# Optimization experiments

Measured on AMD Instinct MI355X. Metric: run time of the kernel, lower is better.

Reference implementation:

```python
import jax, jax.numpy as jnp
import numpy as np

B, C, D = 512, 50000, 256
N_LOADED = 40000


def setup_inputs() -> dict:
    key = jax.random.key(0)
    k1, k2, k3, k4 = jax.random.split(key, 4)
    visual_feats = jax.random.normal(k1, (B, D), dtype=jnp.float32)
    text_feats = jax.random.normal(k2, (C, D), dtype=jnp.float32)
    # sparse multi-hot labels; force class 0 positive for every row so the
    # positive set (intersected with loaded ids) is never empty
    batch_label = (jax.random.uniform(k3, (B, C)) < 0.02).astype(jnp.int32)
    batch_label = batch_label.at[:, 0].set(1)
    # distinct loaded class ids; force id 0 to be loaded
    ids = jax.random.permutation(k4, C)[:N_LOADED].astype(jnp.int32)
    ids = jnp.sort(ids).at[0].set(0)
    return {
        "visual_feats": visual_feats,
        "text_feats": text_feats,
        "batch_label": batch_label,
        "class_ids_loaded": ids,
        "d_space": D,
    }


def reference(visual_feats, text_feats, batch_label, class_ids_loaded, d_space):
    num_classes = text_feats.shape[0]
    # membership mask for loaded class ids (the set() intersection in torch)
    loaded = jnp.zeros((num_classes,), dtype=bool).at[class_ids_loaded].set(True)

    # cosine similarity; note: torch adds 1e-6 eps only to text-feature norms
    v = visual_feats / jnp.linalg.norm(visual_feats, axis=1, keepdims=True)
    t = text_feats / (1e-6 + jnp.linalg.norm(text_feats, axis=1, keepdims=True))
    S = v @ t.T  # [B, C]

    pos = (batch_label != 0) & loaded[None, :]  # ragged positive sets, as mask
    neg = (batch_label == 0) & loaded[None, :]  # ragged negative sets, as mask

    # denominator: sum of exp(sim) over negatives, per row
    denom = jnp.sum(jnp.where(neg, jnp.exp(S), 0.0), axis=1)  # [B]
    n_pos = jnp.sum(pos, axis=1).astype(S.dtype)  # [B]

    # per-row loss: mean over positives of -log(exp(s_p)/denom) = log(denom)-s_p
    per_row = jnp.sum(jnp.where(pos, jnp.log(denom)[:, None] - S, 0.0), axis=1) / n_pos
    return jnp.mean(per_row).reshape(1)
```

## Files before the change

kernel.cpp:

```cpp
#include <hip/hip_runtime.h>
#include <math.h>

#define D_DIM 256
#define TM 128
#define TN 128
#define BK 32
#define NBP 392
#define CBPR 7
#define CBLKS (CBPR * 512)

typedef __attribute__((ext_vector_type(8))) short short8;
typedef __attribute__((ext_vector_type(4))) float floatx4;
typedef unsigned long long u64;

__device__ __forceinline__ unsigned short f2bf(float f) {
    unsigned int u = __float_as_uint(f);
    u += 0x7FFFu + ((u >> 16) & 1u);
    return (unsigned short)(u >> 16);
}

__device__ __forceinline__ void gload16(const void* g, void* lds) {
    __builtin_amdgcn_global_load_lds(
        (const __attribute__((address_space(1))) unsigned int*)g,
        (__attribute__((address_space(3))) unsigned int*)lds, 16, 0, 0);
}

__global__ __launch_bounds__(256) void prep_compress(
    const float* __restrict__ V, const float* __restrict__ T,
    const int* __restrict__ label, const int* __restrict__ ids,
    u64* __restrict__ loadedmask, u64* __restrict__ posmask,
    unsigned short* __restrict__ Vb, unsigned short* __restrict__ Tb,
    float* __restrict__ gaccum, unsigned int* __restrict__ gcount,
    int B, int C, int n_loaded, int WPR) {
    const int bid = blockIdx.x;
    const int tid = threadIdx.x;
    const int lane = tid & 63;

    if (bid < CBLKS) {
        int row = bid / CBPR;
        int sub = bid - row * CBPR;
        int wl  = tid >> 6;
        int w0col = (sub * 4 + wl) * 2048;
        if (w0col >= C) return;
        const int* lp = label + (size_t)row * C;
        int4 v[8];
        #pragma unroll
        for (int r = 0; r < 8; ++r) {
            int c0 = w0col + r * 256 + lane * 4;
            if (c0 < C) {
                v[r] = *(const int4*)(lp + c0);
            } else {
                v[r] = make_int4(0, 0, 0, 0);
            }
        }
        #pragma unroll
        for (int r = 0; r < 8; ++r) {
            unsigned int nib =
                (v[r].x ? 1u : 0u) | (v[r].y ? 2u : 0u) |
                (v[r].z ? 4u : 0u) | (v[r].w ? 8u : 0u);
            u64 wv = (u64)nib << (4 * (lane & 15));
            wv |= __shfl_xor(wv, 1);
            wv |= __shfl_xor(wv, 2);
            wv |= __shfl_xor(wv, 4);
            wv |= __shfl_xor(wv, 8);
            if ((lane & 15) == 0) {
                int wc = ((w0col + r * 256) >> 6) + (lane >> 4);
                if (wc < WPR) posmask[(size_t)row * WPR + wc] = wv;
            }
        }
        return;
    }

    int ptid = (bid - CBLKS) * 256 + tid;
    if (ptid == 0) { *gcount = 0u; *gaccum = 0.f; }
    if (ptid < WPR) {
        int base = ptid << 6;
        int lo = 0, hi = n_loaded;
        while (lo < hi) { int mid = (lo + hi) >> 1; if (ids[mid] < base) lo = mid + 1; else hi = mid; }
        u64 m = 0;
        for (int i = lo; i < n_loaded; ++i) {
            int v = ids[i]; if (v >= base + 64) break;
            m |= 1ull << (v - base);
        }
        loadedmask[ptid] = m;
    }
    int wave = ptid >> 6;
    if (wave >= B + C) return;
    bool isV = wave < B;
    const float* src = isV ? (V + (size_t)wave * D_DIM)
                           : (T + (size_t)(wave - B) * D_DIM);
    float4 x = ((const float4*)src)[lane];
    float ss = x.x * x.x + x.y * x.y + x.z * x.z + x.w * x.w;
    #pragma unroll
    for (int off = 32; off > 0; off >>= 1) ss += __shfl_xor(ss, off);
    float nrm = sqrtf(ss);
    float s = isV ? (1.0f / nrm) : (1.0f / (1e-6f + nrm));
    ushort4 o;
    o.x = f2bf(x.x * s); o.y = f2bf(x.y * s);
    o.z = f2bf(x.z * s); o.w = f2bf(x.w * s);
    unsigned short* dst = isV ? (Vb + (size_t)wave * D_DIM)
                              : (Tb + (size_t)(wave - B) * D_DIM);
    ((ushort4*)dst)[lane] = o;
}

__global__ __launch_bounds__(256) void gemm_fused(
    const unsigned short* __restrict__ Vb, const unsigned short* __restrict__ Tb,
    const u64* __restrict__ posmask, const u64* __restrict__ loadedmask,
    float* __restrict__ denomP, float* __restrict__ posP, int C, int WPR) {
    __shared__ unsigned short As[2][TM * BK];
    __shared__ unsigned short Bs[2][TN * BK];
    __shared__ float sDen[TM], sPos[TM];

    const int tid  = threadIdx.x;
    const int lane = tid & 63;
    const int w    = tid >> 6;
    const int m0 = blockIdx.x * TM;
    const int n0 = blockIdx.y * TN;

    if (tid < TM) { sDen[tid] = 0.f; sPos[tid] = 0.f; }

    const int sra = lane >> 2;
    const int kc  = (lane & 3) * 8;
    int ga  = m0 + w * 32 + sra;
    int gb0 = n0 + w * 32 + sra;
    int gb1 = gb0 + 16;
    if (gb0 >= C) gb0 = C - 1;
    if (gb1 >= C) gb1 = C - 1;
    const unsigned short* gA0 = Vb + (size_t)ga * D_DIM + kc;
    const unsigned short* gA1 = gA0 + (size_t)16 * D_DIM;
    const unsigned short* gB0 = Tb + (size_t)gb0 * D_DIM + kc;
    const unsigned short* gB1 = Tb + (size_t)gb1 * D_DIM + kc;
    const int lofsA = w * 32 * BK;
    const int lofsB = w * 32 * BK;

    const int wm = (w >> 1) * 64;
    const int wn = (w & 1) * 64;
    const int fr = lane & 15;
    const int quad = lane >> 4;

    floatx4 acc[4][4];
    #pragma unroll
    for (int mi = 0; mi < 4; mi++)
        #pragma unroll
        for (int ni = 0; ni < 4; ni++) acc[mi][ni] = (floatx4)0.f;

    gload16(gA0, &As[0][lofsA]);
    gload16(gA1, &As[0][lofsA + 16 * BK]);
    gload16(gB0, &Bs[0][lofsB]);
    gload16(gB1, &Bs[0][lofsB + 16 * BK]);
    __syncthreads();

    #pragma unroll
    for (int kt = 0; kt < D_DIM / BK; ++kt) {
        const int cur = kt & 1;
        if (kt < D_DIM / BK - 1) {
            const int kb = (kt + 1) * BK;
            gload16(gA0 + kb, &As[cur ^ 1][lofsA]);
            gload16(gA1 + kb, &As[cur ^ 1][lofsA + 16 * BK]);
            gload16(gB0 + kb, &Bs[cur ^ 1][lofsB]);
            gload16(gB1 + kb, &Bs[cur ^ 1][lofsB + 16 * BK]);
        }
        short8 af[4], bf[4];
        #pragma unroll
        for (int mi = 0; mi < 4; mi++)
            af[mi] = *(const short8*)&As[cur][(wm + mi * 16 + fr) * BK + quad * 8];
        #pragma unroll
        for (int ni = 0; ni < 4; ni++)
            bf[ni] = *(const short8*)&Bs[cur][(wn + ni * 16 + fr) * BK + quad * 8];
        #pragma unroll
        for (int mi = 0; mi < 4; mi++)
            #pragma unroll
            for (int ni = 0; ni < 4; ni++)
                acc[mi][ni] = __builtin_amdgcn_mfma_f32_16x16x32_bf16(
                    af[mi], bf[ni], acc[mi][ni], 0, 0, 0);
        __syncthreads();
    }

    const int wcol = (n0 + wn) >> 6;
    const u64 loadedw = loadedmask[wcol];
    #pragma unroll
    for (int mi = 0; mi < 4; mi++) {
        #pragma unroll
        for (int i = 0; i < 4; i++) {
            const int mloc = wm + mi * 16 + quad * 4 + i;
            const u64 praw = posmask[(size_t)(m0 + mloc) * WPR + wcol];
            const u64 posw = praw & loadedw;
            const u64 negw = loadedw & ~praw;
            float den = 0.f, pos = 0.f;
            #pragma unroll
            for (int ni = 0; ni < 4; ni++) {
                const float s = acc[mi][ni][i];
                const int bit = ni * 16 + fr;
                if ((negw >> bit) & 1) den += __expf(s);
                if ((posw >> bit) & 1) pos += s;
            }
            #pragma unroll
            for (int off = 8; off >= 1; off >>= 1) {
                den += __shfl_xor(den, off);
                pos += __shfl_xor(pos, off);
            }
            if (fr == 0) {
                if (den != 0.f) atomicAdd(&sDen[mloc], den);
                if (pos != 0.f) atomicAdd(&sPos[mloc], pos);
            }
        }
    }
    __syncthreads();
    if (tid < TM) {
        denomP[(size_t)(m0 + tid) * NBP + blockIdx.y] = sDen[tid];
        posP[(size_t)(m0 + tid) * NBP + blockIdx.y]   = sPos[tid];
    }
}

__global__ void reduce_rows(const float* __restrict__ denomP, const float* __restrict__ posP,
                            const u64* __restrict__ posmask, const u64* __restrict__ loadedmask,
                            float* __restrict__ gaccum, unsigned int* __restrict__ gcount,
                            float* __restrict__ out, int B, int NB, int WPR) {
    __shared__ float bsum[4];
    int wv   = threadIdx.x >> 6;
    int row  = blockIdx.x * 4 + wv;
    int lane = threadIdx.x & 63;
    float den = 0.f, pos = 0.f;
    int cnt = 0;
    if (row < B) {
        for (int bn = lane; bn < NB; bn += 64) {
            den += denomP[(size_t)row * NBP + bn];
            pos += posP[(size_t)row * NBP + bn];
        }
        for (int j = lane; j < WPR; j += 64)
            cnt += __popcll(posmask[(size_t)row * WPR + j] & loadedmask[j]);
        #pragma unroll
        for (int off = 32; off > 0; off >>= 1) {
            den += __shfl_xor(den, off);
            pos += __shfl_xor(pos, off);
            cnt += __shfl_xor(cnt, off);
        }
    }
    if (lane == 0) bsum[wv] = (row < B) ? (logf(den) - pos / (float)cnt) : 0.f;
    __syncthreads();
    if (threadIdx.x == 0) {
        float s = bsum[0] + bsum[1] + bsum[2] + bsum[3];
        atomicAdd(gaccum, s);
        __threadfence();
        unsigned int old = atomicAdd(gcount, 1u);
        if (old == gridDim.x - 1) {
            float tot = atomicAdd(gaccum, 0.0f);
            out[0] = tot / (float)B;
        }
    }
}

extern "C" void kernel_launch(void* const* d_in, const int* in_sizes, int n_in,
                              void* d_out, int out_size, void* d_ws, size_t ws_size,
                              hipStream_t stream) {
    const float* V     = (const float*)d_in[0];
    const float* T     = (const float*)d_in[1];
    const int*   label = (const int*)d_in[2];
    const int*   ids   = (const int*)d_in[3];
    int B = in_sizes[0] / D_DIM;
    int C = in_sizes[1] / D_DIM;
    int n_loaded = in_sizes[3];
    int WPR = (C + 63) >> 6;
    int NB  = (C + TN - 1) / TN;

    char* ws = (char*)d_ws;
    float*        gaccum = (float*)(ws + 0);
    unsigned int* gcount = (unsigned int*)(ws + 8);
    u64*   loadedmask = (u64*)(ws + 2048);
    u64*   posmask    = (u64*)(ws + 8320);
    unsigned short* Vb = (unsigned short*)(ws + 3211392);
    unsigned short* Tb = (unsigned short*)(ws + 3473536);
    float* denomP  = (float*)(ws + 29073536);
    float* posP    = (float*)(ws + 29876352);

    int prep_blocks = ((B + C) * 64 + 255) / 256;
    prep_compress<<<CBLKS + prep_blocks, 256, 0, stream>>>(
        V, T, label, ids, loadedmask, posmask, Vb, Tb, gaccum, gcount,
        B, C, n_loaded, WPR);

    dim3 grid(B / TM, NB);
    gemm_fused<<<grid, 256, 0, stream>>>(Vb, Tb, posmask, loadedmask,
                                         denomP, posP, C, WPR);

    reduce_rows<<<(B + 3) / 4, 256, 0, stream>>>(denomP, posP, posmask, loadedmask,
                                                 gaccum, gcount, (float*)d_out, B, NB, WPR);
}
```

Measured before the change: 263.9 us.

## Fuse label bitmask compression into GEMM epilogue, count positives per tile

Removes the separate pass that compressed the int32 label matrix into a per-row bitmask. Each GEMM block now reads its own 128x128 label tile directly, with one row per lane, builds the 64-bit positive mask and broadcasts it by shuffle. The block also accumulates the positive count with atomics, so the reduce kernel no longer rescans masks. This saves the bitmask write and re-read plus a large prep grid. In exchange, the GEMM gains strided label loads (each lane reads a different row) and extra global atomics.

New measurement: 273.3 us. +3.6%, slower.

```diff
diff --git a/kernel.cpp b/kernel.cpp
--- a/kernel.cpp
+++ b/kernel.cpp
@@ -6,8 +6,6 @@
 #define TN 128
 #define BK 32
 #define NBP 392
-#define CBPR 7
-#define CBLKS (CBPR * 512)
 
 typedef __attribute__((ext_vector_type(8))) short short8;
 typedef __attribute__((ext_vector_type(4))) float floatx4;
@@ -25,54 +23,18 @@
         (__attribute__((address_space(3))) unsigned int*)lds, 16, 0, 0);
 }
 
-__global__ __launch_bounds__(256) void prep_compress(
+__global__ __launch_bounds__(256) void prep_rows(
     const float* __restrict__ V, const float* __restrict__ T,
-    const int* __restrict__ label, const int* __restrict__ ids,
-    u64* __restrict__ loadedmask, u64* __restrict__ posmask,
+    const int* __restrict__ ids,
+    u64* __restrict__ loadedmask, unsigned int* __restrict__ cntG,
     unsigned short* __restrict__ Vb, unsigned short* __restrict__ Tb,
     float* __restrict__ gaccum, unsigned int* __restrict__ gcount,
     int B, int C, int n_loaded, int WPR) {
-    const int bid = blockIdx.x;
-    const int tid = threadIdx.x;
+    const int tid  = threadIdx.x;
     const int lane = tid & 63;
-
-    if (bid < CBLKS) {
-        int row = bid / CBPR;
-        int sub = bid - row * CBPR;
-        int wl  = tid >> 6;
-        int w0col = (sub * 4 + wl) * 2048;
-        if (w0col >= C) return;
-        const int* lp = label + (size_t)row * C;
-        int4 v[8];
-        #pragma unroll
-        for (int r = 0; r < 8; ++r) {
-            int c0 = w0col + r * 256 + lane * 4;
-            if (c0 < C) {
-                v[r] = *(const int4*)(lp + c0);
-            } else {
-                v[r] = make_int4(0, 0, 0, 0);
-            }
-        }
-        #pragma unroll
-        for (int r = 0; r < 8; ++r) {
-            unsigned int nib =
-                (v[r].x ? 1u : 0u) | (v[r].y ? 2u : 0u) |
-                (v[r].z ? 4u : 0u) | (v[r].w ? 8u : 0u);
-            u64 wv = (u64)nib << (4 * (lane & 15));
-            wv |= __shfl_xor(wv, 1);
-            wv |= __shfl_xor(wv, 2);
-            wv |= __shfl_xor(wv, 4);
-            wv |= __shfl_xor(wv, 8);
-            if ((lane & 15) == 0) {
-                int wc = ((w0col + r * 256) >> 6) + (lane >> 4);
-                if (wc < WPR) posmask[(size_t)row * WPR + wc] = wv;
-            }
-        }
-        return;
-    }
-
-    int ptid = (bid - CBLKS) * 256 + tid;
+    int ptid = blockIdx.x * 256 + tid;
     if (ptid == 0) { *gcount = 0u; *gaccum = 0.f; }
+    if (ptid < B) cntG[ptid] = 0u;
     if (ptid < WPR) {
         int base = ptid << 6;
         int lo = 0, hi = n_loaded;
@@ -105,11 +67,13 @@
 
 __global__ __launch_bounds__(256) void gemm_fused(
     const unsigned short* __restrict__ Vb, const unsigned short* __restrict__ Tb,
-    const u64* __restrict__ posmask, const u64* __restrict__ loadedmask,
-    float* __restrict__ denomP, float* __restrict__ posP, int C, int WPR) {
+    const int* __restrict__ label, const u64* __restrict__ loadedmask,
+    float* __restrict__ denomP, float* __restrict__ posP,
+    unsigned int* __restrict__ cntG, int C, int WPR) {
     __shared__ unsigned short As[2][TM * BK];
     __shared__ unsigned short Bs[2][TN * BK];
     __shared__ float sDen[TM], sPos[TM];
+    __shared__ int sCnt[TM];
 
     const int tid  = threadIdx.x;
     const int lane = tid & 63;
@@ -117,7 +81,32 @@
     const int m0 = blockIdx.x * TM;
     const int n0 = blockIdx.y * TN;
 
-    if (tid < TM) { sDen[tid] = 0.f; sPos[tid] = 0.f; }
+    if (tid < TM) { sDen[tid] = 0.f; sPos[tid] = 0.f; sCnt[tid] = 0; }
+
+    const int wm = (w >> 1) * 64;
+    const int wn = (w & 1) * 64;
+    const int fr = lane & 15;
+    const int quad = lane >> 4;
+
+    const u64 loadedw = loadedmask[(n0 + wn) >> 6];
+    const int* lp = label + (size_t)(m0 + wm + lane) * C;
+    const int nBase = n0 + wn;
+    u64 praw = 0;
+    #pragma unroll
+    for (int k = 0; k < 16; ++k) {
+        const int col0 = nBase + 4 * k;
+        unsigned int nib = 0;
+        if (col0 + 3 < C) {
+            int4 v = *(const int4*)(lp + col0);
+            nib = (v.x ? 1u : 0u) | (v.y ? 2u : 0u) | (v.z ? 4u : 0u) | (v.w ? 8u : 0u);
+        } else {
+            if (col0 + 0 < C && lp[col0 + 0]) nib |= 1u;
+            if (col0 + 1 < C && lp[col0 + 1]) nib |= 2u;
+            if (col0 + 2 < C && lp[col0 + 2]) nib |= 4u;
+            if (col0 + 3 < C && lp[col0 + 3]) nib |= 8u;
+        }
+        praw |= (u64)nib << (4 * k);
+    }
 
     const int sra = lane >> 2;
     const int kc  = (lane & 3) * 8;
@@ -133,11 +122,6 @@
     const int lofsA = w * 32 * BK;
     const int lofsB = w * 32 * BK;
 
-    const int wm = (w >> 1) * 64;
-    const int wn = (w & 1) * 64;
-    const int fr = lane & 15;
-    const int quad = lane >> 4;
-
     floatx4 acc[4][4];
     #pragma unroll
     for (int mi = 0; mi < 4; mi++)
@@ -176,16 +160,16 @@
         __syncthreads();
     }
 
-    const int wcol = (n0 + wn) >> 6;
-    const u64 loadedw = loadedmask[wcol];
+    atomicAdd(&sCnt[wm + lane], (int)__popcll(praw & loadedw));
     #pragma unroll
     for (int mi = 0; mi < 4; mi++) {
         #pragma unroll
         for (int i = 0; i < 4; i++) {
-            const int mloc = wm + mi * 16 + quad * 4 + i;
-            const u64 praw = posmask[(size_t)(m0 + mloc) * WPR + wcol];
-            const u64 posw = praw & loadedw;
-            const u64 negw = loadedw & ~praw;
+            const int rloc = mi * 16 + quad * 4 + i;
+            const int mloc = wm + rloc;
+            const u64 pr = __shfl(praw, rloc);
+            const u64 posw = pr & loadedw;
+            const u64 negw = loadedw & ~pr;
             float den = 0.f, pos = 0.f;
             #pragma unroll
             for (int ni = 0; ni < 4; ni++) {
@@ -209,34 +193,31 @@
     if (tid < TM) {
         denomP[(size_t)(m0 + tid) * NBP + blockIdx.y] = sDen[tid];
         posP[(size_t)(m0 + tid) * NBP + blockIdx.y]   = sPos[tid];
+        if (sCnt[tid]) atomicAdd(&cntG[m0 + tid], (unsigned int)sCnt[tid]);
     }
 }
 
 __global__ void reduce_rows(const float* __restrict__ denomP, const float* __restrict__ posP,
-                            const u64* __restrict__ posmask, const u64* __restrict__ loadedmask,
+                            const unsigned int* __restrict__ cntG,
                             float* __restrict__ gaccum, unsigned int* __restrict__ gcount,
-                            float* __restrict__ out, int B, int NB, int WPR) {
+                            float* __restrict__ out, int B, int NB) {
     __shared__ float bsum[4];
     int wv   = threadIdx.x >> 6;
     int row  = blockIdx.x * 4 + wv;
     int lane = threadIdx.x & 63;
     float den = 0.f, pos = 0.f;
-    int cnt = 0;
     if (row < B) {
         for (int bn = lane; bn < NB; bn += 64) {
             den += denomP[(size_t)row * NBP + bn];
             pos += posP[(size_t)row * NBP + bn];
         }
-        for (int j = lane; j < WPR; j += 64)
-            cnt += __popcll(posmask[(size_t)row * WPR + j] & loadedmask[j]);
         #pragma unroll
         for (int off = 32; off > 0; off >>= 1) {
             den += __shfl_xor(den, off);
             pos += __shfl_xor(pos, off);
-            cnt += __shfl_xor(cnt, off);
-        }
-    }
-    if (lane == 0) bsum[wv] = (row < B) ? (logf(den) - pos / (float)cnt) : 0.f;
+        }
+    }
+    if (lane == 0) bsum[wv] = (row < B) ? (logf(den) - pos / (float)cntG[row]) : 0.f;
     __syncthreads();
     if (threadIdx.x == 0) {
         float s = bsum[0] + bsum[1] + bsum[2] + bsum[3];
@@ -266,22 +247,22 @@
     char* ws = (char*)d_ws;
     float*        gaccum = (float*)(ws + 0);
     unsigned int* gcount = (unsigned int*)(ws + 8);
-    u64*   loadedmask = (u64*)(ws + 2048);
-    u64*   posmask    = (u64*)(ws + 8320);
-    unsigned short* Vb = (unsigned short*)(ws + 3211392);
-    unsigned short* Tb = (unsigned short*)(ws + 3473536);
-    float* denomP  = (float*)(ws + 29073536);
-    float* posP    = (float*)(ws + 29876352);
+    unsigned int* cntG   = (unsigned int*)(ws + 64);
+    u64*   loadedmask = (u64*)(ws + 4096);
+    unsigned short* Vb = (unsigned short*)(ws + 16384);
+    unsigned short* Tb = (unsigned short*)(ws + 278528);
+    float* denomP  = (float*)(ws + 25878528);
+    float* posP    = (float*)(ws + 26681344);
 
     int prep_blocks = ((B + C) * 64 + 255) / 256;
-    prep_compress<<<CBLKS + prep_blocks, 256, 0, stream>>>(
-        V, T, label, ids, loadedmask, posmask, Vb, Tb, gaccum, gcount,
+    prep_rows<<<prep_blocks, 256, 0, stream>>>(
+        V, T, ids, loadedmask, cntG, Vb, Tb, gaccum, gcount,
         B, C, n_loaded, WPR);
 
     dim3 grid(B / TM, NB);
-    gemm_fused<<<grid, 256, 0, stream>>>(Vb, Tb, posmask, loadedmask,
-                                         denomP, posP, C, WPR);
-
-    reduce_rows<<<(B + 3) / 4, 256, 0, stream>>>(denomP, posP, posmask, loadedmask,
-                                                 gaccum, gcount, (float*)d_out, B, NB, WPR);
-}
+    gemm_fused<<<grid, 256, 0, stream>>>(Vb, Tb, label, loadedmask,
+                                         denomP, posP, cntG, C, WPR);
+
+    reduce_rows<<<(B + 3) / 4, 256, 0, stream>>>(denomP, posP, cntG,
+                                                 gaccum, gcount, (float*)d_out, B, NB);
+}
```
